# Optimization experiments

Measured on AMD Instinct MI355X. Metric: run time of the kernel, lower is better.

Reference implementation:

```python
import jax, jax.numpy as jnp
import numpy as np

NUM_HEADS = 16  # init kwarg num_attention_heads


def setup_inputs() -> dict:
    key = jax.random.key(0)
    k1, k2, k3, k4 = jax.random.split(key, 4)
    B, T, E = 2, 2048, 1024
    query = jax.random.normal(k1, (B, T, E), dtype=jnp.float32)
    key_t = jax.random.normal(k2, (B, T, E), dtype=jnp.float32)
    value = jax.random.normal(k3, (B, T, E), dtype=jnp.float32)
    # final output projection (nn.Linear(hidden, hidden, bias=False)); torch stores [out,in]
    W_out = jax.random.normal(k4, (E, E), dtype=jnp.float32) * 0.02
    return {"query": query, "key": key_t, "value": value, "W_out": W_out}


def reference(query, key, value, W_out):
    # NOTE: in the source, the per-head q_i/k_i/v_i linear projections are
    # overwritten by reshapes of the raw inputs, so the qs/ks/vs weights are
    # dead code. Every head computes identical output; mean over heads is a
    # no-op. We reproduce that exact math here.
    B, T, E = query.shape
    H = NUM_HEADS
    d = E // H  # head_dim; also d_k used in the 1/sqrt(d_k) scaling

    def split_heads(x):  # [B,T,E] -> [B,H,T,d]
        return x.reshape(B, T, H, d).transpose(0, 2, 1, 3)

    q = split_heads(query)
    k = split_heads(key)
    v = split_heads(value)

    scale = jnp.sqrt(jnp.asarray(d, dtype=jnp.float32))
    scores = jnp.einsum('bhtd,bhsd->bhts', q, k) / scale  # [B,H,T,T]
    attn = jax.nn.softmax(scores, axis=-1)
    head = jnp.einsum('bhts,bhsd->bhtd', attn, v)         # [B,H,T,d]
    head = head.transpose(0, 2, 1, 3).reshape(B, T, E)    # concat heads

    # mean over H identical head outputs == head; final linear (no bias)
    outputs = head @ W_out.T                              # [B,T,E]
    # mean over H identical attention maps == attn, returned as [B*H,T,T]
    attention = attn.reshape(B * H, T, T)
    return outputs, attention
```

## Files before the change

### kernel.cpp

```cpp
#include <hip/hip_runtime.h>
#include <hip/hip_fp16.h>

#define B_NUM  2
#define T_DIM  2048
#define E_DIM  1024
#define H_NUM  16
#define D_HEAD 64
#define BH_NUM (B_NUM * H_NUM)
#define NT     (T_DIM / 64)

using half8  = __attribute__((ext_vector_type(8))) _Float16;
using half4v = __attribute__((ext_vector_type(4))) _Float16;
using f32x4  = __attribute__((ext_vector_type(4))) float;

#define AS1 __attribute__((address_space(1)))
#define AS3 __attribute__((address_space(3)))

#define QSCALE 0.18033688011112042f

#define BAR_VM(N)                                                       \
    do {                                                                \
        asm volatile("s_waitcnt vmcnt(" #N ")" ::: "memory");           \
        __builtin_amdgcn_s_barrier();                                   \
        __builtin_amdgcn_sched_barrier(0);                              \
    } while (0)

__device__ __forceinline__ void bar_plain() {
    __builtin_amdgcn_s_barrier();
    __builtin_amdgcn_sched_barrier(0);
}

__global__ void cast_f16_kernel(const float* __restrict__ in,
                                _Float16* __restrict__ out, int n4) {
    int stride = gridDim.x * blockDim.x;
    for (int i = blockIdx.x * blockDim.x + threadIdx.x; i < n4; i += stride) {
        float4 v = reinterpret_cast<const float4*>(in)[i];
        half4v h;
        h[0] = (_Float16)v.x; h[1] = (_Float16)v.y;
        h[2] = (_Float16)v.z; h[3] = (_Float16)v.w;
        reinterpret_cast<half4v*>(out)[i] = h;
    }
}

__global__ void transpose_v_kernel(const float* __restrict__ V,
                                   _Float16* __restrict__ Vt) {
    __shared__ float tile[64][65];
    int s0 = blockIdx.x * 64;
    int bh = blockIdx.y;
    int b = bh >> 4, h = bh & 15;
    int t = threadIdx.x;

    int row = t >> 2;
    int c0  = (t & 3) * 16;
    const float* src = V + ((size_t)(b * T_DIM + s0 + row)) * E_DIM + h * D_HEAD + c0;
#pragma unroll
    for (int j = 0; j < 16; j += 4) {
        float4 v = *reinterpret_cast<const float4*>(src + j);
        tile[row][c0 + j + 0] = v.x;
        tile[row][c0 + j + 1] = v.y;
        tile[row][c0 + j + 2] = v.z;
        tile[row][c0 + j + 3] = v.w;
    }
    __syncthreads();

    int d  = t >> 2;
    int sc = (t & 3) * 16;
    half8 h0, h1;
#pragma unroll
    for (int j = 0; j < 8; ++j) {
        h0[j] = (_Float16)tile[sc + j][d];
        h1[j] = (_Float16)tile[sc + 8 + j][d];
    }
    _Float16* dst = Vt + ((size_t)(bh * D_HEAD + d)) * T_DIM + s0 + sc;
    *reinterpret_cast<half8*>(dst)     = h0;
    *reinterpret_cast<half8*>(dst + 8) = h1;
}

__device__ __forceinline__ void stage_gl(const _Float16* __restrict__ g,
                                         size_t stride, _Float16* lds,
                                         int w, int lane) {
    int r0 = lane >> 3;
    int c  = (lane & 7) ^ r0;
#pragma unroll
    for (int j = 0; j < 2; ++j) {
        int r = (w + 4 * j) * 8 + r0;
        const _Float16* src = g + (size_t)r * stride + c * 8;
        _Float16* dst = lds + (w + 4 * j) * 512;
        __builtin_amdgcn_global_load_lds((const AS1 void*)src, (AS3 void*)dst,
                                         16, 0, 0);
    }
}

__device__ __forceinline__ half8 read_frag64(const _Float16* lds, int row, int chunk) {
    int csw = chunk ^ (row & 7);
    return *reinterpret_cast<const half8*>(lds + row * 64 + csw * 8);
}

__global__ __launch_bounds__(256) void attn_kernel(
        const float* __restrict__ Q, const _Float16* __restrict__ Kh,
        const _Float16* __restrict__ Vt, float* __restrict__ attn_out,
        _Float16* __restrict__ head_h) {
    __shared__ __align__(16) _Float16 kbuf[2][64 * 64];
    __shared__ __align__(16) _Float16 vbuf[2][64 * 64];
    __shared__ __align__(16) _Float16 pbuf[4][16 * 64];

    int tid  = threadIdx.x;
    int wq   = tid >> 6;
    int lane = tid & 63;
    int l15  = lane & 15;
    int lg   = lane >> 4;

    int flat = blockIdx.x;
    int bh   = (flat & 7) * 4 + (flat >> 8);
    int qt   = (flat >> 3) & 31;
    int q0   = qt * 64;
    int b = bh >> 4, h = bh & 15;

    const float* qsrc = Q + ((size_t)(b * T_DIM + q0 + wq * 16 + l15)) * E_DIM + h * D_HEAD;
    half8 qfrag[2];
#pragma unroll
    for (int ks = 0; ks < 2; ++ks) {
        float4 a0 = *reinterpret_cast<const float4*>(qsrc + (lg + 4 * ks) * 8);
        float4 a1 = *reinterpret_cast<const float4*>(qsrc + (lg + 4 * ks) * 8 + 4);
        qfrag[ks][0] = (_Float16)(a0.x * QSCALE); qfrag[ks][1] = (_Float16)(a0.y * QSCALE);
        qfrag[ks][2] = (_Float16)(a0.z * QSCALE); qfrag[ks][3] = (_Float16)(a0.w * QSCALE);
        qfrag[ks][4] = (_Float16)(a1.x * QSCALE); qfrag[ks][5] = (_Float16)(a1.y * QSCALE);
        qfrag[ks][6] = (_Float16)(a1.z * QSCALE); qfrag[ks][7] = (_Float16)(a1.w * QSCALE);
    }

    const _Float16* kg = Kh + ((size_t)b * T_DIM) * E_DIM + h * D_HEAD;
    const _Float16* vg = Vt + (size_t)bh * D_HEAD * T_DIM;

#define P1TILE(KB)                                                             \
    {                                                                          \
        f32x4 acc[4];                                                          \
        _Pragma("unroll")                                                      \
        for (int ct = 0; ct < 4; ++ct) acc[ct] = (f32x4){0.f, 0.f, 0.f, 0.f};  \
        _Pragma("unroll")                                                      \
        for (int ks = 0; ks < 2; ++ks)                                         \
            _Pragma("unroll")                                                  \
            for (int ct = 0; ct < 4; ++ct) {                                   \
                half8 kf = read_frag64((KB), ct * 16 + l15, lg + 4 * ks);      \
                acc[ct] = __builtin_amdgcn_mfma_f32_16x16x32_f16(              \
                    kf, qfrag[ks], acc[ct], 0, 0, 0);                          \
            }                                                                  \
        _Pragma("unroll")                                                      \
        for (int ct = 0; ct < 4; ++ct)                                         \
            _Pragma("unroll")                                                  \
            for (int r = 0; r < 4; ++r)                                        \
                lsum += __builtin_amdgcn_exp2f(acc[ct][r]);                    \
    }

    float lsum = 0.0f;
    int cur = 0;
    stage_gl(kg, E_DIM, kbuf[0], wq, lane);
    for (int t = 0; t < NT - 1; ++t) {
        stage_gl(kg + (size_t)(t + 1) * 64 * E_DIM, E_DIM, kbuf[cur ^ 1], wq, lane);
        BAR_VM(2);
        P1TILE(kbuf[cur]);
        bar_plain();
        cur ^= 1;
    }
    BAR_VM(0);
    P1TILE(kbuf[cur]);

    lsum += __shfl_xor(lsum, 16);
    lsum += __shfl_xor(lsum, 32);
    float rl = 1.0f / lsum;

    f32x4 oacc[4];
#pragma unroll
    for (int cd = 0; cd < 4; ++cd) oacc[cd] = (f32x4){0.f, 0.f, 0.f, 0.f};

    float* ab = attn_out + (size_t)bh * T_DIM * T_DIM;
    _Float16* pw = pbuf[wq];
    int myq = q0 + wq * 16 + l15;

    bar_plain();

    cur = 0;
    stage_gl(kg, E_DIM, kbuf[0], wq, lane);
    stage_gl(vg, T_DIM, vbuf[0], wq, lane);
    for (int t = 0; t < NT; ++t) {
        if (t < NT - 1) {
            stage_gl(kg + (size_t)(t + 1) * 64 * E_DIM, E_DIM, kbuf[cur ^ 1], wq, lane);
            stage_gl(vg + (t + 1) * 64, T_DIM, vbuf[cur ^ 1], wq, lane);
        }
        if (t == 0)           BAR_VM(4);
        else if (t < NT - 1)  BAR_VM(8);
        else                  BAR_VM(4);
        const _Float16* kb = kbuf[cur];
        const _Float16* vb = vbuf[cur];

        f32x4 acc[4];
#pragma unroll
        for (int ct = 0; ct < 4; ++ct) acc[ct] = (f32x4){0.f, 0.f, 0.f, 0.f};
#pragma unroll
        for (int ks = 0; ks < 2; ++ks)
#pragma unroll
            for (int ct = 0; ct < 4; ++ct) {
                half8 kf = read_frag64(kb, ct * 16 + l15, lg + 4 * ks);
                acc[ct] = __builtin_amdgcn_mfma_f32_16x16x32_f16(kf, qfrag[ks], acc[ct], 0, 0, 0);
            }

        float* abrow = ab + (size_t)myq * T_DIM + t * 64 + lg * 4;
#pragma unroll
        for (int ct = 0; ct < 4; ++ct) {
            f32x4 p;
            p[0] = __builtin_amdgcn_exp2f(acc[ct][0]) * rl;
            p[1] = __builtin_amdgcn_exp2f(acc[ct][1]) * rl;
            p[2] = __builtin_amdgcn_exp2f(acc[ct][2]) * rl;
            p[3] = __builtin_amdgcn_exp2f(acc[ct][3]) * rl;
            *reinterpret_cast<f32x4*>(abrow + ct * 16) = p;
            half4v ph;
            ph[0] = (_Float16)p[0]; ph[1] = (_Float16)p[1];
            ph[2] = (_Float16)p[2]; ph[3] = (_Float16)p[3];
            int cc = (ct * 4 + lg) ^ l15;
            *reinterpret_cast<half4v*>(pw + l15 * 64 + cc * 4) = ph;
        }

#pragma unroll
        for (int ks = 0; ks < 2; ++ks) {
            int c0 = 2 * (lg + 4 * ks);
            half4v lo = *reinterpret_cast<const half4v*>(pw + l15 * 64 + ((c0)     ^ l15) * 4);
            half4v hi = *reinterpret_cast<const half4v*>(pw + l15 * 64 + ((c0 + 1) ^ l15) * 4);
            half8 pa;
            pa[0] = lo[0]; pa[1] = lo[1]; pa[2] = lo[2]; pa[3] = lo[3];
            pa[4] = hi[0]; pa[5] = hi[1]; pa[6] = hi[2]; pa[7] = hi[3];
#pragma unroll
            for (int cd = 0; cd < 4; ++cd) {
                half8 vf = read_frag64(vb, cd * 16 + l15, lg + 4 * ks);
                oacc[cd] = __builtin_amdgcn_mfma_f32_16x16x32_f16(pa, vf, oacc[cd], 0, 0, 0);
            }
        }
        bar_plain();
        cur ^= 1;
    }

    _Float16* hw = head_h + ((size_t)(b * T_DIM + q0 + wq * 16)) * E_DIM + h * D_HEAD;
#pragma unroll
    for (int cd = 0; cd < 4; ++cd)
#pragma unroll
        for (int r = 0; r < 4; ++r) {
            int qm = lg * 4 + r;
            hw[(size_t)qm * E_DIM + cd * 16 + l15] = (_Float16)oacc[cd][r];
        }
#undef P1TILE
}

__global__ __launch_bounds__(256) void proj_kernel(
        const _Float16* __restrict__ A, const _Float16* __restrict__ Wh,
        float* __restrict__ out) {
    __shared__ __align__(16) _Float16 abuf[2][64 * 64];
    __shared__ __align__(16) _Float16 bbuf[2][64 * 64];

    int tid  = threadIdx.x;
    int wq   = tid >> 6;
    int lane = tid & 63;
    int l15  = lane & 15;
    int lg   = lane >> 4;

    int m0 = blockIdx.x * 64;
    int n0 = blockIdx.y * 64;

    f32x4 acc[4];
#pragma unroll
    for (int ct = 0; ct < 4; ++ct) acc[ct] = (f32x4){0.f, 0.f, 0.f, 0.f};

    int cur = 0;
    stage_gl(A  + (size_t)m0 * E_DIM, E_DIM, abuf[0], wq, lane);
    stage_gl(Wh + (size_t)n0 * E_DIM, E_DIM, bbuf[0], wq, lane);
    for (int t = 0; t < E_DIM / 64; ++t) {
        if (t + 1 < E_DIM / 64) {
            stage_gl(A  + (size_t)m0 * E_DIM + (t + 1) * 64, E_DIM, abuf[cur ^ 1], wq, lane);
            stage_gl(Wh + (size_t)n0 * E_DIM + (t + 1) * 64, E_DIM, bbuf[cur ^ 1], wq, lane);
            BAR_VM(4);
        } else {
            BAR_VM(0);
        }
#pragma unroll
        for (int ks = 0; ks < 2; ++ks) {
            half8 hf = read_frag64(abuf[cur], wq * 16 + l15, lg + 4 * ks);
#pragma unroll
            for (int ct = 0; ct < 4; ++ct) {
                half8 wf = read_frag64(bbuf[cur], ct * 16 + l15, lg + 4 * ks);
                acc[ct] = __builtin_amdgcn_mfma_f32_16x16x32_f16(wf, hf, acc[ct], 0, 0, 0);
            }
        }
        bar_plain();
        cur ^= 1;
    }

    float* orow = out + (size_t)(m0 + wq * 16 + l15) * E_DIM + n0 + lg * 4;
#pragma unroll
    for (int ct = 0; ct < 4; ++ct) {
        f32x4 o;
        o[0] = acc[ct][0]; o[1] = acc[ct][1]; o[2] = acc[ct][2]; o[3] = acc[ct][3];
        *reinterpret_cast<f32x4*>(orow + ct * 16) = o;
    }
}

extern "C" void kernel_launch(void* const* d_in, const int* in_sizes, int n_in,
                              void* d_out, int out_size, void* d_ws, size_t ws_size,
                              hipStream_t stream) {
    const float* q = (const float*)d_in[0];
    const float* k = (const float*)d_in[1];
    const float* v = (const float*)d_in[2];
    const float* w = (const float*)d_in[3];

    float* outs = (float*)d_out;
    float* attn = outs + (size_t)B_NUM * T_DIM * E_DIM;

    char* ws = (char*)d_ws;
    _Float16* Kh = (_Float16*)(ws);
    _Float16* Vt = (_Float16*)(ws + (size_t)(8  << 20));
    _Float16* Wh = (_Float16*)(ws + (size_t)(16 << 20));
    _Float16* Hh = (_Float16*)(ws + (size_t)(18 << 20));

    int nqkv4 = B_NUM * T_DIM * E_DIM / 4;
    int nw4   = E_DIM * E_DIM / 4;

    cast_f16_kernel<<<1024, 256, 0, stream>>>(k, Kh, nqkv4);
    cast_f16_kernel<<<512, 256, 0, stream>>>(w, Wh, nw4);
    transpose_v_kernel<<<dim3(T_DIM / 64, BH_NUM), 256, 0, stream>>>(v, Vt);
    attn_kernel<<<NT * BH_NUM, 256, 0, stream>>>(q, Kh, Vt, attn, Hh);
    proj_kernel<<<dim3((B_NUM * T_DIM) / 64, E_DIM / 64), 256, 0, stream>>>(Hh, Wh, outs);
}
```

Before: 223.6 us.

## Process two query tiles per block, fusing second tile's row-sum pass into first tile's output pass

Each block now handles 128 query rows as two 64-row halves. The first-pass row-sum for the second half is computed inside the first half's probability/PV loop, reusing the same staged K tiles, so one full sweep over K is saved per pair of tiles. K/V traffic drops from three sweeps per 64 rows to five per 128 rows. The trade-off is half as many blocks (512), more registers for extra Q fragments, and more serial work per block, which may hurt occupancy or load balance.

```diff
diff --git a/kernel.cpp b/kernel.cpp
--- a/kernel.cpp
+++ b/kernel.cpp
@@ -111,27 +111,32 @@
     int lg   = lane >> 4;
 
     int flat = blockIdx.x;
-    int bh   = (flat & 7) * 4 + (flat >> 8);
-    int qt   = (flat >> 3) & 31;
-    int q0   = qt * 64;
+    int i    = flat >> 3;
+    int bh   = (flat & 7) * 4 + (i >> 4);
+    int q0   = (i & 15) * 128;
     int b = bh >> 4, h = bh & 15;
 
-    const float* qsrc = Q + ((size_t)(b * T_DIM + q0 + wq * 16 + l15)) * E_DIM + h * D_HEAD;
-    half8 qfrag[2];
-#pragma unroll
-    for (int ks = 0; ks < 2; ++ks) {
-        float4 a0 = *reinterpret_cast<const float4*>(qsrc + (lg + 4 * ks) * 8);
-        float4 a1 = *reinterpret_cast<const float4*>(qsrc + (lg + 4 * ks) * 8 + 4);
-        qfrag[ks][0] = (_Float16)(a0.x * QSCALE); qfrag[ks][1] = (_Float16)(a0.y * QSCALE);
-        qfrag[ks][2] = (_Float16)(a0.z * QSCALE); qfrag[ks][3] = (_Float16)(a0.w * QSCALE);
-        qfrag[ks][4] = (_Float16)(a1.x * QSCALE); qfrag[ks][5] = (_Float16)(a1.y * QSCALE);
-        qfrag[ks][6] = (_Float16)(a1.z * QSCALE); qfrag[ks][7] = (_Float16)(a1.w * QSCALE);
+    half8 qfA[2], qfB[2];
+#pragma unroll
+    for (int half_ = 0; half_ < 2; ++half_) {
+        const float* qsrc = Q + ((size_t)(b * T_DIM + q0 + half_ * 64 + wq * 16 + l15)) * E_DIM
+                          + h * D_HEAD;
+        half8* qf = half_ ? qfB : qfA;
+#pragma unroll
+        for (int ks = 0; ks < 2; ++ks) {
+            float4 a0 = *reinterpret_cast<const float4*>(qsrc + (lg + 4 * ks) * 8);
+            float4 a1 = *reinterpret_cast<const float4*>(qsrc + (lg + 4 * ks) * 8 + 4);
+            qf[ks][0] = (_Float16)(a0.x * QSCALE); qf[ks][1] = (_Float16)(a0.y * QSCALE);
+            qf[ks][2] = (_Float16)(a0.z * QSCALE); qf[ks][3] = (_Float16)(a0.w * QSCALE);
+            qf[ks][4] = (_Float16)(a1.x * QSCALE); qf[ks][5] = (_Float16)(a1.y * QSCALE);
+            qf[ks][6] = (_Float16)(a1.z * QSCALE); qf[ks][7] = (_Float16)(a1.w * QSCALE);
+        }
     }
 
     const _Float16* kg = Kh + ((size_t)b * T_DIM) * E_DIM + h * D_HEAD;
     const _Float16* vg = Vt + (size_t)bh * D_HEAD * T_DIM;
 
-#define P1TILE(KB)                                                             \
+#define P1TILE(KB, QF, LS)                                                     \
     {                                                                          \
         f32x4 acc[4];                                                          \
         _Pragma("unroll")                                                      \
@@ -142,39 +147,90 @@
             for (int ct = 0; ct < 4; ++ct) {                                   \
                 half8 kf = read_frag64((KB), ct * 16 + l15, lg + 4 * ks);      \
                 acc[ct] = __builtin_amdgcn_mfma_f32_16x16x32_f16(              \
-                    kf, qfrag[ks], acc[ct], 0, 0, 0);                          \
+                    kf, (QF)[ks], acc[ct], 0, 0, 0);                           \
             }                                                                  \
         _Pragma("unroll")                                                      \
         for (int ct = 0; ct < 4; ++ct)                                         \
             _Pragma("unroll")                                                  \
             for (int r = 0; r < 4; ++r)                                        \
-                lsum += __builtin_amdgcn_exp2f(acc[ct][r]);                    \
-    }
-
-    float lsum = 0.0f;
+                (LS) += __builtin_amdgcn_exp2f(acc[ct][r]);                    \
+    }
+
+#define P2TILE(KB, VB, QF, RL, ABROW, OACC)                                    \
+    {                                                                          \
+        f32x4 acc[4];                                                          \
+        _Pragma("unroll")                                                      \
+        for (int ct = 0; ct < 4; ++ct) acc[ct] = (f32x4){0.f, 0.f, 0.f, 0.f};  \
+        _Pragma("unroll")                                                      \
+        for (int ks = 0; ks < 2; ++ks)                                         \
+            _Pragma("unroll")                                                  \
+            for (int ct = 0; ct < 4; ++ct) {                                   \
+                half8 kf = read_frag64((KB), ct * 16 + l15, lg + 4 * ks);      \
+                acc[ct] = __builtin_amdgcn_mfma_f32_16x16x32_f16(              \
+                    kf, (QF)[ks], acc[ct], 0, 0, 0);                           \
+            }                                                                  \
+        _Pragma("unroll")                                                      \
+        for (int ct = 0; ct < 4; ++ct) {                                       \
+            f32x4 p;                                                           \
+            p[0] = __builtin_amdgcn_exp2f(acc[ct][0]) * (RL);                  \
+            p[1] = __builtin_amdgcn_exp2f(acc[ct][1]) * (RL);                  \
+            p[2] = __builtin_amdgcn_exp2f(acc[ct][2]) * (RL);                  \
+            p[3] = __builtin_amdgcn_exp2f(acc[ct][3]) * (RL);                  \
+            *reinterpret_cast<f32x4*>((ABROW) + ct * 16) = p;                  \
+            half4v ph;                                                         \
+            ph[0] = (_Float16)p[0]; ph[1] = (_Float16)p[1];                    \
+            ph[2] = (_Float16)p[2]; ph[3] = (_Float16)p[3];                    \
+            int cc = (ct * 4 + lg) ^ l15;                                      \
+            *reinterpret_cast<half4v*>(pw + l15 * 64 + cc * 4) = ph;           \
+        }                                                                      \
+    }
+
+#define PVTILE(VB, OACC)                                                       \
+    {                                                                          \
+        _Pragma("unroll")                                                      \
+        for (int ks = 0; ks < 2; ++ks) {                                       \
+            int c0 = 2 * (lg + 4 * ks);                                        \
+            half4v lo = *reinterpret_cast<const half4v*>(                      \
+                pw + l15 * 64 + ((c0)     ^ l15) * 4);                         \
+            half4v hi = *reinterpret_cast<const half4v*>(                      \
+                pw + l15 * 64 + ((c0 + 1) ^ l15) * 4);                         \
+            half8 pa;                                                          \
+            pa[0] = lo[0]; pa[1] = lo[1]; pa[2] = lo[2]; pa[3] = lo[3];        \
+            pa[4] = hi[0]; pa[5] = hi[1]; pa[6] = hi[2]; pa[7] = hi[3];        \
+            _Pragma("unroll")                                                  \
+            for (int cd = 0; cd < 4; ++cd) {                                   \
+                half8 vf = read_frag64((VB), cd * 16 + l15, lg + 4 * ks);      \
+                (OACC)[cd] = __builtin_amdgcn_mfma_f32_16x16x32_f16(           \
+                    pa, vf, (OACC)[cd], 0, 0, 0);                              \
+            }                                                                  \
+        }                                                                      \
+    }
+
+    float* ab = attn_out + (size_t)bh * T_DIM * T_DIM;
+    _Float16* pw = pbuf[wq];
+    int myqA = q0 + wq * 16 + l15;
+    int myqB = myqA + 64;
+
+    float lsumA = 0.0f, lsumB = 0.0f;
     int cur = 0;
     stage_gl(kg, E_DIM, kbuf[0], wq, lane);
     for (int t = 0; t < NT - 1; ++t) {
         stage_gl(kg + (size_t)(t + 1) * 64 * E_DIM, E_DIM, kbuf[cur ^ 1], wq, lane);
         BAR_VM(2);
-        P1TILE(kbuf[cur]);
+        P1TILE(kbuf[cur], qfA, lsumA);
         bar_plain();
         cur ^= 1;
     }
     BAR_VM(0);
-    P1TILE(kbuf[cur]);
-
-    lsum += __shfl_xor(lsum, 16);
-    lsum += __shfl_xor(lsum, 32);
-    float rl = 1.0f / lsum;
+    P1TILE(kbuf[cur], qfA, lsumA);
+
+    lsumA += __shfl_xor(lsumA, 16);
+    lsumA += __shfl_xor(lsumA, 32);
+    float rlA = 1.0f / lsumA;
 
     f32x4 oacc[4];
 #pragma unroll
     for (int cd = 0; cd < 4; ++cd) oacc[cd] = (f32x4){0.f, 0.f, 0.f, 0.f};
-
-    float* ab = attn_out + (size_t)bh * T_DIM * T_DIM;
-    _Float16* pw = pbuf[wq];
-    int myq = q0 + wq * 16 + l15;
 
     bar_plain();
 
@@ -192,60 +248,62 @@
         const _Float16* kb = kbuf[cur];
         const _Float16* vb = vbuf[cur];
 
-        f32x4 acc[4];
-#pragma unroll
-        for (int ct = 0; ct < 4; ++ct) acc[ct] = (f32x4){0.f, 0.f, 0.f, 0.f};
-#pragma unroll
-        for (int ks = 0; ks < 2; ++ks)
-#pragma unroll
-            for (int ct = 0; ct < 4; ++ct) {
-                half8 kf = read_frag64(kb, ct * 16 + l15, lg + 4 * ks);
-                acc[ct] = __builtin_amdgcn_mfma_f32_16x16x32_f16(kf, qfrag[ks], acc[ct], 0, 0, 0);
-            }
-
-        float* abrow = ab + (size_t)myq * T_DIM + t * 64 + lg * 4;
-#pragma unroll
-        for (int ct = 0; ct < 4; ++ct) {
-            f32x4 p;
-            p[0] = __builtin_amdgcn_exp2f(acc[ct][0]) * rl;
-            p[1] = __builtin_amdgcn_exp2f(acc[ct][1]) * rl;
-            p[2] = __builtin_amdgcn_exp2f(acc[ct][2]) * rl;
-            p[3] = __builtin_amdgcn_exp2f(acc[ct][3]) * rl;
-            *reinterpret_cast<f32x4*>(abrow + ct * 16) = p;
-            half4v ph;
-            ph[0] = (_Float16)p[0]; ph[1] = (_Float16)p[1];
-            ph[2] = (_Float16)p[2]; ph[3] = (_Float16)p[3];
-            int cc = (ct * 4 + lg) ^ l15;
-            *reinterpret_cast<half4v*>(pw + l15 * 64 + cc * 4) = ph;
-        }
-
-#pragma unroll
-        for (int ks = 0; ks < 2; ++ks) {
-            int c0 = 2 * (lg + 4 * ks);
-            half4v lo = *reinterpret_cast<const half4v*>(pw + l15 * 64 + ((c0)     ^ l15) * 4);
-            half4v hi = *reinterpret_cast<const half4v*>(pw + l15 * 64 + ((c0 + 1) ^ l15) * 4);
-            half8 pa;
-            pa[0] = lo[0]; pa[1] = lo[1]; pa[2] = lo[2]; pa[3] = lo[3];
-            pa[4] = hi[0]; pa[5] = hi[1]; pa[6] = hi[2]; pa[7] = hi[3];
-#pragma unroll
-            for (int cd = 0; cd < 4; ++cd) {
-                half8 vf = read_frag64(vb, cd * 16 + l15, lg + 4 * ks);
-                oacc[cd] = __builtin_amdgcn_mfma_f32_16x16x32_f16(pa, vf, oacc[cd], 0, 0, 0);
-            }
-        }
+        float* abrowA = ab + (size_t)myqA * T_DIM + t * 64 + lg * 4;
+        P2TILE(kb, vb, qfA, rlA, abrowA, oacc);
+        P1TILE(kb, qfB, lsumB);
+        PVTILE(vb, oacc);
         bar_plain();
         cur ^= 1;
     }
 
-    _Float16* hw = head_h + ((size_t)(b * T_DIM + q0 + wq * 16)) * E_DIM + h * D_HEAD;
-#pragma unroll
-    for (int cd = 0; cd < 4; ++cd)
-#pragma unroll
-        for (int r = 0; r < 4; ++r) {
-            int qm = lg * 4 + r;
-            hw[(size_t)qm * E_DIM + cd * 16 + l15] = (_Float16)oacc[cd][r];
-        }
+    lsumB += __shfl_xor(lsumB, 16);
+    lsumB += __shfl_xor(lsumB, 32);
+    float rlB = 1.0f / lsumB;
+
+    {
+        _Float16* hw = head_h + ((size_t)(b * T_DIM + q0 + wq * 16)) * E_DIM + h * D_HEAD;
+#pragma unroll
+        for (int cd = 0; cd < 4; ++cd)
+#pragma unroll
+            for (int r = 0; r < 4; ++r)
+                hw[(size_t)(lg * 4 + r) * E_DIM + cd * 16 + l15] = (_Float16)oacc[cd][r];
+    }
+
+#pragma unroll
+    for (int cd = 0; cd < 4; ++cd) oacc[cd] = (f32x4){0.f, 0.f, 0.f, 0.f};
+
+    cur = 0;
+    stage_gl(kg, E_DIM, kbuf[0], wq, lane);
+    stage_gl(vg, T_DIM, vbuf[0], wq, lane);
+    for (int t = 0; t < NT; ++t) {
+        if (t < NT - 1) {
+            stage_gl(kg + (size_t)(t + 1) * 64 * E_DIM, E_DIM, kbuf[cur ^ 1], wq, lane);
+            stage_gl(vg + (t + 1) * 64, T_DIM, vbuf[cur ^ 1], wq, lane);
+        }
+        if (t == 0)           BAR_VM(4);
+        else if (t < NT - 1)  BAR_VM(8);
+        else                  BAR_VM(4);
+        const _Float16* kb = kbuf[cur];
+        const _Float16* vb = vbuf[cur];
+
+        float* abrowB = ab + (size_t)myqB * T_DIM + t * 64 + lg * 4;
+        P2TILE(kb, vb, qfB, rlB, abrowB, oacc);
+        PVTILE(vb, oacc);
+        bar_plain();
+        cur ^= 1;
+    }
+
+    {
+        _Float16* hw = head_h + ((size_t)(b * T_DIM + q0 + 64 + wq * 16)) * E_DIM + h * D_HEAD;
+#pragma unroll
+        for (int cd = 0; cd < 4; ++cd)
+#pragma unroll
+            for (int r = 0; r < 4; ++r)
+                hw[(size_t)(lg * 4 + r) * E_DIM + cd * 16 + l15] = (_Float16)oacc[cd][r];
+    }
 #undef P1TILE
+#undef P2TILE
+#undef PVTILE
 }
 
 __global__ __launch_bounds__(256) void proj_kernel(
@@ -323,6 +381,6 @@
     cast_f16_kernel<<<1024, 256, 0, stream>>>(k, Kh, nqkv4);
     cast_f16_kernel<<<512, 256, 0, stream>>>(w, Wh, nw4);
     transpose_v_kernel<<<dim3(T_DIM / 64, BH_NUM), 256, 0, stream>>>(v, Vt);
-    attn_kernel<<<NT * BH_NUM, 256, 0, stream>>>(q, Kh, Vt, attn, Hh);
+    attn_kernel<<<(T_DIM / 128) * BH_NUM, 256, 0, stream>>>(q, Kh, Vt, attn, Hh);
     proj_kernel<<<dim3((B_NUM * T_DIM) / 64, E_DIM / 64), 256, 0, stream>>>(Hh, Wh, outs);
 }
```

Result: no change. 228.0 us (+2.0%).
